# Optimization experiments

Measured on AMD Instinct MI355X. Metric: run time of the kernel, lower is better.

The kernel has to match this reference:

```python
import jax, jax.numpy as jnp
import numpy as np


def setup_inputs() -> dict:
    key = jax.random.key(0)
    k1, k2 = jax.random.split(key)
    z = jax.random.normal(k1, (16, 128, 32, 32), dtype=jnp.float32)
    e = jax.random.normal(k2, (8192, 128), dtype=jnp.float32)
    log_sigma = jnp.zeros((1,), dtype=jnp.float32)  # init_log_sigma = 0.0
    return {"z": z, "e": e, "log_sigma": log_sigma}


def reference(z, e, log_sigma):
    # z: [B, C, H, W] latents; e: [M, C] codebook; log_sigma: [1]
    B, C, H, W = z.shape
    zf = jnp.transpose(z, (0, 2, 3, 1)).reshape(-1, C)  # [N, C]
    N = zf.shape[0]
    M = e.shape[0]
    T = 1.0  # latent_temp default

    # squared L2 distance via expanded dot products: ||z||^2 + ||e||^2 - 2 z.e
    z_sq = jnp.sum(zf * zf, axis=1, keepdims=True)          # [N, 1]
    e_sq = jnp.sum(e * e, axis=1)[None, :]                  # [1, M]
    dist = jnp.maximum(z_sq + e_sq - 2.0 * (zf @ e.T), 0.0)  # [N, M]

    alpha = -1.0 / (2.0 * jnp.exp(log_sigma[0]) ** 2)
    A = alpha * dist / T                                     # [N, M]

    # np.log(np.e) == 1.0 in the original
    const = 0.5 * C * (2.0 * log_sigma - 1.0)                # [1]
    lse1_loss = -jnp.mean(T * jax.nn.logsumexp(A, axis=1)) + const + jnp.log(float(M))
    lse2_loss = -jnp.mean(T * jax.nn.logsumexp(A, axis=0)) + const + jnp.log(float(N))
    return lse1_loss, lse2_loss
```

## Files before the change

### kernel.cpp

```cpp
#include <hip/hip_runtime.h>
#include <hip/hip_bf16.h>

typedef unsigned short u16;
typedef __attribute__((ext_vector_type(8))) short short8;
typedef __attribute__((ext_vector_type(4))) float float4v;

#define N_ROWS 16384
#define M_COLS 8192
#define KDIM   128
#define SHIFT  64.0f

__device__ inline u16 f2bf(float f) {
  unsigned u = __builtin_bit_cast(unsigned, f);
  unsigned r = (u + 0x7fffu + ((u >> 16) & 1u)) >> 16;
  return (u16)r;
}

__global__ void prep_z(const float* __restrict__ z, u16* __restrict__ zf,
                       float* __restrict__ zsq) {
  const int b = blockIdx.x >> 5, h = blockIdx.x & 31;
  __shared__ float tile[128 * 33];
  __shared__ float psum[8][32];
  const float* src = z + ((size_t)b * 128 * 32 + h) * 32;
  for (int idx = threadIdx.x; idx < 4096; idx += 256) {
    int c = idx >> 5, w = idx & 31;
    tile[c * 33 + w] = src[c * 1024 + w];
  }
  __syncthreads();
  {
    int w = threadIdx.x & 31, cg = threadIdx.x >> 5;
    float s = 0.f;
#pragma unroll
    for (int cc = 0; cc < 16; ++cc) {
      float v = tile[(cg * 16 + cc) * 33 + w];
      s = fmaf(v, v, s);
    }
    psum[cg][w] = s;
  }
  for (int idx = threadIdx.x; idx < 512; idx += 256) {
    int w = idx >> 4, g = idx & 15;
    short8 v;
#pragma unroll
    for (int cc = 0; cc < 8; ++cc) v[cc] = (short)f2bf(tile[(g * 8 + cc) * 33 + w]);
    *(short8*)&zf[((size_t)b * 1024 + h * 32 + w) * 128 + g * 8] = v;
  }
  __syncthreads();
  if (threadIdx.x < 32) {
    int w = threadIdx.x;
    float s = 0.f;
#pragma unroll
    for (int cg = 0; cg < 8; ++cg) s += psum[cg][w];
    zsq[b * 1024 + h * 32 + w] = s;
  }
}

__global__ void prep_e(const float* __restrict__ e, u16* __restrict__ ef,
                       float* __restrict__ esq) {
  const int gw = (blockIdx.x * 256 + threadIdx.x) >> 6;
  const int ln = threadIdx.x & 63;
  for (int r = gw; r < M_COLS; r += 256) {
    float2 v = *(const float2*)&e[r * 128 + ln * 2];
    unsigned pk = (unsigned)f2bf(v.x) | ((unsigned)f2bf(v.y) << 16);
    *(unsigned*)&ef[r * 128 + ln * 2] = pk;
    float s = fmaf(v.x, v.x, v.y * v.y);
#pragma unroll
    for (int sh = 1; sh < 64; sh <<= 1) s += __shfl_xor(s, sh);
    if (ln == 0) esq[r] = s;
  }
}

__global__ __launch_bounds__(1024, 4) void gemm_lse(
    const u16* __restrict__ zf, const u16* __restrict__ ef,
    const float* __restrict__ zsq, const float* __restrict__ esq,
    const float* __restrict__ log_sigma,
    float* __restrict__ rowsum, float* __restrict__ colsum) {
  __shared__ __align__(16) u16 zt[256 * 128];
  __shared__ __align__(16) u16 et[256 * 128];
  const int tid = threadIdx.x;
  const int ln = tid & 63, wv = tid >> 6;
  const int wr = wv >> 2, wc = wv & 3;
  const int l15 = ln & 15, q = ln >> 4;
  const int bx = blockIdx.x, by = blockIdx.y;

  const u16* zsrc = zf + (size_t)by * (256 * 128);
  const u16* esrc = ef + (size_t)bx * (256 * 128);
#pragma unroll
  for (int it = 0; it < 4; ++it) {
    int u = it * 1024 + tid;
    int r = u >> 4, p = u & 15;
    int g = p ^ (r & 15);
    int soff = r * 128 + g * 8;
    int lbase = (it * 1024 + wv * 64) * 8;
    __builtin_amdgcn_global_load_lds(
        (const __attribute__((address_space(1))) unsigned int*)(zsrc + soff),
        (__attribute__((address_space(3))) unsigned int*)(zt + lbase), 16, 0, 0);
    __builtin_amdgcn_global_load_lds(
        (const __attribute__((address_space(1))) unsigned int*)(esrc + soff),
        (__attribute__((address_space(3))) unsigned int*)(et + lbase), 16, 0, 0);
  }

  float4v acc[4][4];
#pragma unroll
  for (int i = 0; i < 4; ++i)
#pragma unroll
    for (int j = 0; j < 4; ++j) acc[i][j] = (float4v){0.f, 0.f, 0.f, 0.f};

  __syncthreads();

#pragma unroll
  for (int kk = 0; kk < 4; ++kk) {
    short8 af[4], bfr[4];
    const int poff = ((kk * 4 + q) ^ l15) * 8;
#pragma unroll
    for (int i = 0; i < 4; ++i)
      af[i] = *(const short8*)(zt + (wr * 64 + i * 16 + l15) * 128 + poff);
#pragma unroll
    for (int j = 0; j < 4; ++j)
      bfr[j] = *(const short8*)(et + (wc * 64 + j * 16 + l15) * 128 + poff);
#pragma unroll
    for (int i = 0; i < 4; ++i)
#pragma unroll
      for (int j = 0; j < 4; ++j)
        acc[i][j] = __builtin_amdgcn_mfma_f32_16x16x32_bf16(af[i], bfr[j], acc[i][j], 0, 0, 0);
  }

  const float lsv = log_sigma[0];
  const float sg = __expf(lsv);
  const float alpha = -0.5f / (sg * sg);
  const float L2E = 1.44269504088896f;
  const float ca = alpha * L2E, cb = SHIFT * L2E, m2ca = -2.0f * ca;

  float4v zb[4];
  float eb[4];
#pragma unroll
  for (int i = 0; i < 4; ++i) {
    float4v zs = *(const float4v*)(zsq + by * 256 + wr * 64 + i * 16 + q * 4);
#pragma unroll
    for (int r = 0; r < 4; ++r) zb[i][r] = fmaf(ca, zs[r], cb);
  }
#pragma unroll
  for (int j = 0; j < 4; ++j) eb[j] = ca * esq[bx * 256 + wc * 64 + j * 16 + l15];

  float rs[4][4] = {};
  float cs[4] = {};
#pragma unroll
  for (int i = 0; i < 4; ++i) {
#pragma unroll
    for (int j = 0; j < 4; ++j) {
      float ex0, ex1, ex2, ex3;
      {
        float arg = fmaf(acc[i][j][0], m2ca, zb[i][0] + eb[j]);
        ex0 = __builtin_amdgcn_exp2f(arg);
      }
      {
        float arg = fmaf(acc[i][j][1], m2ca, zb[i][1] + eb[j]);
        ex1 = __builtin_amdgcn_exp2f(arg);
      }
      {
        float arg = fmaf(acc[i][j][2], m2ca, zb[i][2] + eb[j]);
        ex2 = __builtin_amdgcn_exp2f(arg);
      }
      {
        float arg = fmaf(acc[i][j][3], m2ca, zb[i][3] + eb[j]);
        ex3 = __builtin_amdgcn_exp2f(arg);
      }
      rs[i][0] += ex0; rs[i][1] += ex1; rs[i][2] += ex2; rs[i][3] += ex3;
      cs[j] += (ex0 + ex1) + (ex2 + ex3);
    }
  }
#pragma unroll
  for (int i = 0; i < 4; ++i)
#pragma unroll
    for (int r = 0; r < 4; ++r)
      for (int s = 1; s < 16; s <<= 1) rs[i][r] += __shfl_xor(rs[i][r], s);
#pragma unroll
  for (int j = 0; j < 4; ++j) {
    cs[j] += __shfl_xor(cs[j], 16);
    cs[j] += __shfl_xor(cs[j], 32);
  }

  __syncthreads();
  float* rbuf = (float*)zt;
  float* cbuf = rbuf + 1024;
  if (l15 == 0) {
#pragma unroll
    for (int i = 0; i < 4; ++i)
#pragma unroll
      for (int r = 0; r < 4; ++r)
        rbuf[wc * 256 + wr * 64 + i * 16 + q * 4 + r] = rs[i][r];
  }
  if (q == 0) {
#pragma unroll
    for (int j = 0; j < 4; ++j)
      cbuf[wr * 256 + wc * 64 + j * 16 + l15] = cs[j];
  }
  __syncthreads();
  if (tid < 256) {
    atomicAdd(&rowsum[by * 256 + tid],
              (rbuf[tid] + rbuf[256 + tid]) + (rbuf[512 + tid] + rbuf[768 + tid]));
  } else if (tid < 512) {
    int t = tid - 256;
    atomicAdd(&colsum[bx * 256 + t],
              (cbuf[t] + cbuf[256 + t]) + (cbuf[512 + t] + cbuf[768 + t]));
  }
}

__global__ void finalize(const float* __restrict__ rowsum, const float* __restrict__ colsum,
                         const float* __restrict__ log_sigma, float* __restrict__ out) {
  const int tid = threadIdx.x;
  const bool rows = (blockIdx.x == 0);
  const int n = rows ? N_ROWS : M_COLS;
  const float* buf = rows ? rowsum : colsum;
  double part = 0.0;
  for (int i = tid; i < n; i += 1024) part += (double)logf(buf[i]);
  __shared__ double red[1024];
  red[tid] = part;
  __syncthreads();
  for (int s = 512; s > 0; s >>= 1) {
    if (tid < s) red[tid] += red[tid + s];
    __syncthreads();
  }
  if (tid == 0) {
    float lsv = log_sigma[0];
    float cst = 0.5f * 128.0f * (2.0f * lsv - 1.0f);
    float lother = rows ? logf((float)M_COLS) : logf((float)N_ROWS);
    out[blockIdx.x] = (float)(-(red[0] / n - (double)SHIFT)) + cst + lother;
  }
}

extern "C" void kernel_launch(void* const* d_in, const int* in_sizes, int n_in,
                              void* d_out, int out_size, void* d_ws, size_t ws_size,
                              hipStream_t stream) {
  const float* z  = (const float*)d_in[0];
  const float* e  = (const float*)d_in[1];
  const float* ls = (const float*)d_in[2];
  float* out = (float*)d_out;
  char* ws = (char*)d_ws;
  u16*  zf     = (u16*)ws;
  u16*  ef     = (u16*)(ws + (4u << 20));
  float* zsq   = (float*)(ws + (6u << 20));
  float* esq   = (float*)(ws + (6u << 20) + 65536);
  float* rowsum = (float*)(ws + (6u << 20) + 65536 + 32768);
  float* colsum = (float*)(ws + (6u << 20) + 65536 + 32768 + 65536);

  hipMemsetAsync(rowsum, 0, 65536 + 32768, stream);
  prep_z<<<dim3(512), dim3(256), 0, stream>>>(z, zf, zsq);
  prep_e<<<dim3(64), dim3(256), 0, stream>>>(e, ef, esq);
  gemm_lse<<<dim3(32, 64), dim3(1024), 0, stream>>>(zf, ef, zsq, esq, ls, rowsum, colsum);
  finalize<<<dim3(2), dim3(1024), 0, stream>>>(rowsum, colsum, ls, out);
}
```

Measured before the change: 169.4 us.

## Restructure GEMM-LSE into register-resident z stripes with double-buffered codebook tiles

The two prep kernels are merged into one launch. The main kernel now keeps each block's 256 z rows in registers and streams 64-column codebook tiles through double-buffered LDS using async global-to-LDS loads. Global atomics and the memset are replaced by per-split row partials and per-stripe column partials, which a two-stage finalize reduces. This gives 512 blocks of 256 threads instead of 2048 blocks of 1024 threads, trading parallelism for operand reuse and less atomic traffic. It adds larger partial buffers and an extra kernel launch.

Measured after the change: 151.7 us. 10.4% less time.

```diff
diff --git a/kernel.cpp b/kernel.cpp
--- a/kernel.cpp
+++ b/kernel.cpp
@@ -9,6 +9,9 @@
 #define M_COLS 8192
 #define KDIM   128
 #define SHIFT  64.0f
+#define STRIPES 64
+#define SPLITS  8
+#define TILES   16
 
 __device__ inline u16 f2bf(float f) {
   unsigned u = __builtin_bit_cast(unsigned, f);
@@ -16,113 +19,81 @@
   return (u16)r;
 }
 
-__global__ void prep_z(const float* __restrict__ z, u16* __restrict__ zf,
-                       float* __restrict__ zsq) {
-  const int b = blockIdx.x >> 5, h = blockIdx.x & 31;
-  __shared__ float tile[128 * 33];
-  __shared__ float psum[8][32];
-  const float* src = z + ((size_t)b * 128 * 32 + h) * 32;
-  for (int idx = threadIdx.x; idx < 4096; idx += 256) {
-    int c = idx >> 5, w = idx & 31;
-    tile[c * 33 + w] = src[c * 1024 + w];
-  }
-  __syncthreads();
-  {
-    int w = threadIdx.x & 31, cg = threadIdx.x >> 5;
-    float s = 0.f;
-#pragma unroll
-    for (int cc = 0; cc < 16; ++cc) {
-      float v = tile[(cg * 16 + cc) * 33 + w];
-      s = fmaf(v, v, s);
-    }
-    psum[cg][w] = s;
-  }
-  for (int idx = threadIdx.x; idx < 512; idx += 256) {
-    int w = idx >> 4, g = idx & 15;
-    short8 v;
-#pragma unroll
-    for (int cc = 0; cc < 8; ++cc) v[cc] = (short)f2bf(tile[(g * 8 + cc) * 33 + w]);
-    *(short8*)&zf[((size_t)b * 1024 + h * 32 + w) * 128 + g * 8] = v;
-  }
-  __syncthreads();
-  if (threadIdx.x < 32) {
-    int w = threadIdx.x;
-    float s = 0.f;
-#pragma unroll
-    for (int cg = 0; cg < 8; ++cg) s += psum[cg][w];
-    zsq[b * 1024 + h * 32 + w] = s;
-  }
-}
-
-__global__ void prep_e(const float* __restrict__ e, u16* __restrict__ ef,
-                       float* __restrict__ esq) {
-  const int gw = (blockIdx.x * 256 + threadIdx.x) >> 6;
-  const int ln = threadIdx.x & 63;
-  for (int r = gw; r < M_COLS; r += 256) {
-    float2 v = *(const float2*)&e[r * 128 + ln * 2];
-    unsigned pk = (unsigned)f2bf(v.x) | ((unsigned)f2bf(v.y) << 16);
-    *(unsigned*)&ef[r * 128 + ln * 2] = pk;
-    float s = fmaf(v.x, v.x, v.y * v.y);
-#pragma unroll
-    for (int sh = 1; sh < 64; sh <<= 1) s += __shfl_xor(s, sh);
-    if (ln == 0) esq[r] = s;
-  }
-}
-
-__global__ __launch_bounds__(1024, 4) void gemm_lse(
+__global__ void prep(const float* __restrict__ z, const float* __restrict__ e,
+                     u16* __restrict__ zf, u16* __restrict__ ef,
+                     float* __restrict__ zsq, float* __restrict__ esq) {
+  if (blockIdx.x < 512) {
+    const int b = blockIdx.x >> 5, h = blockIdx.x & 31;
+    __shared__ float tile[128 * 33];
+    __shared__ float psum[8][32];
+    const float* src = z + ((size_t)b * 128 * 32 + h) * 32;
+    for (int idx = threadIdx.x; idx < 4096; idx += 256) {
+      int c = idx >> 5, w = idx & 31;
+      tile[c * 33 + w] = src[c * 1024 + w];
+    }
+    __syncthreads();
+    {
+      int w = threadIdx.x & 31, cg = threadIdx.x >> 5;
+      float s = 0.f;
+#pragma unroll
+      for (int cc = 0; cc < 16; ++cc) {
+        float v = tile[(cg * 16 + cc) * 33 + w];
+        s = fmaf(v, v, s);
+      }
+      psum[cg][w] = s;
+    }
+    for (int idx = threadIdx.x; idx < 512; idx += 256) {
+      int w = idx >> 4, g = idx & 15;
+      short8 v;
+#pragma unroll
+      for (int cc = 0; cc < 8; ++cc) v[cc] = (short)f2bf(tile[(g * 8 + cc) * 33 + w]);
+      *(short8*)&zf[((size_t)b * 1024 + h * 32 + w) * 128 + g * 8] = v;
+    }
+    __syncthreads();
+    if (threadIdx.x < 32) {
+      int w = threadIdx.x;
+      float s = 0.f;
+#pragma unroll
+      for (int cg = 0; cg < 8; ++cg) s += psum[cg][w];
+      zsq[b * 1024 + h * 32 + w] = s;
+    }
+  } else {
+    const int gw = ((blockIdx.x - 512) * 256 + threadIdx.x) >> 6;
+    const int ln = threadIdx.x & 63;
+    for (int r = gw; r < M_COLS; r += 256) {
+      float2 v = *(const float2*)&e[r * 128 + ln * 2];
+      unsigned pk = (unsigned)f2bf(v.x) | ((unsigned)f2bf(v.y) << 16);
+      *(unsigned*)&ef[r * 128 + ln * 2] = pk;
+      float s = fmaf(v.x, v.x, v.y * v.y);
+#pragma unroll
+      for (int sh = 1; sh < 64; sh <<= 1) s += __shfl_xor(s, sh);
+      if (ln == 0) esq[r] = s;
+    }
+  }
+}
+
+__global__ __launch_bounds__(256, 2) void gemm_lse(
     const u16* __restrict__ zf, const u16* __restrict__ ef,
     const float* __restrict__ zsq, const float* __restrict__ esq,
     const float* __restrict__ log_sigma,
-    float* __restrict__ rowsum, float* __restrict__ colsum) {
-  __shared__ __align__(16) u16 zt[256 * 128];
-  __shared__ __align__(16) u16 et[256 * 128];
+    float* __restrict__ rpart, float* __restrict__ cpart) {
+  __shared__ __align__(16) u16 et[2][64 * 128];
+  __shared__ float colacc[1024];
   const int tid = threadIdx.x;
   const int ln = tid & 63, wv = tid >> 6;
-  const int wr = wv >> 2, wc = wv & 3;
   const int l15 = ln & 15, q = ln >> 4;
-  const int bx = blockIdx.x, by = blockIdx.y;
-
-  const u16* zsrc = zf + (size_t)by * (256 * 128);
-  const u16* esrc = ef + (size_t)bx * (256 * 128);
-#pragma unroll
-  for (int it = 0; it < 4; ++it) {
-    int u = it * 1024 + tid;
-    int r = u >> 4, p = u & 15;
-    int g = p ^ (r & 15);
-    int soff = r * 128 + g * 8;
-    int lbase = (it * 1024 + wv * 64) * 8;
-    __builtin_amdgcn_global_load_lds(
-        (const __attribute__((address_space(1))) unsigned int*)(zsrc + soff),
-        (__attribute__((address_space(3))) unsigned int*)(zt + lbase), 16, 0, 0);
-    __builtin_amdgcn_global_load_lds(
-        (const __attribute__((address_space(1))) unsigned int*)(esrc + soff),
-        (__attribute__((address_space(3))) unsigned int*)(et + lbase), 16, 0, 0);
-  }
-
-  float4v acc[4][4];
+  const int stripe = blockIdx.x, split = blockIdx.y;
+  const int colbase = split * 1024;
+
+  for (int i = tid; i < 1024; i += 256) colacc[i] = 0.f;
+
+  short8 af[4][4];
 #pragma unroll
   for (int i = 0; i < 4; ++i)
 #pragma unroll
-    for (int j = 0; j < 4; ++j) acc[i][j] = (float4v){0.f, 0.f, 0.f, 0.f};
-
-  __syncthreads();
-
-#pragma unroll
-  for (int kk = 0; kk < 4; ++kk) {
-    short8 af[4], bfr[4];
-    const int poff = ((kk * 4 + q) ^ l15) * 8;
-#pragma unroll
-    for (int i = 0; i < 4; ++i)
-      af[i] = *(const short8*)(zt + (wr * 64 + i * 16 + l15) * 128 + poff);
-#pragma unroll
-    for (int j = 0; j < 4; ++j)
-      bfr[j] = *(const short8*)(et + (wc * 64 + j * 16 + l15) * 128 + poff);
-#pragma unroll
-    for (int i = 0; i < 4; ++i)
-#pragma unroll
-      for (int j = 0; j < 4; ++j)
-        acc[i][j] = __builtin_amdgcn_mfma_f32_16x16x32_bf16(af[i], bfr[j], acc[i][j], 0, 0, 0);
-  }
+    for (int kk = 0; kk < 4; ++kk)
+      af[i][kk] = *(const short8*)(zf +
+          (size_t)(stripe * 256 + wv * 64 + i * 16 + l15) * 128 + kk * 32 + q * 8);
 
   const float lsv = log_sigma[0];
   const float sg = __expf(lsv);
@@ -130,101 +101,164 @@
   const float L2E = 1.44269504088896f;
   const float ca = alpha * L2E, cb = SHIFT * L2E, m2ca = -2.0f * ca;
 
-  float4v zb[4];
-  float eb[4];
+  float4v zbl[4];
 #pragma unroll
   for (int i = 0; i < 4; ++i) {
-    float4v zs = *(const float4v*)(zsq + by * 256 + wr * 64 + i * 16 + q * 4);
-#pragma unroll
-    for (int r = 0; r < 4; ++r) zb[i][r] = fmaf(ca, zs[r], cb);
-  }
-#pragma unroll
-  for (int j = 0; j < 4; ++j) eb[j] = ca * esq[bx * 256 + wc * 64 + j * 16 + l15];
-
-  float rs[4][4] = {};
-  float cs[4] = {};
-#pragma unroll
-  for (int i = 0; i < 4; ++i) {
+    float4v zs = *(const float4v*)(zsq + stripe * 256 + wv * 64 + i * 16 + q * 4);
+#pragma unroll
+    for (int r = 0; r < 4; ++r) zbl[i][r] = fmaf(ca, zs[r], cb);
+  }
+
+  float2 rs2[4][2];
+#pragma unroll
+  for (int i = 0; i < 4; ++i)
+#pragma unroll
+    for (int p = 0; p < 2; ++p) rs2[i][p] = make_float2(0.f, 0.f);
+
+#define STAGE(tt)                                                              \
+  do {                                                                         \
+    const u16* efb = ef + (size_t)(colbase + (tt) * 64) * 128;                 \
+    u16* dstb = et[(tt) & 1];                                                  \
+    _Pragma("unroll")                                                          \
+    for (int it = 0; it < 4; ++it) {                                           \
+      int u = it * 256 + tid;                                                  \
+      int r = u >> 4, p_ = u & 15;                                             \
+      int g = p_ ^ (r & 15);                                                   \
+      __builtin_amdgcn_global_load_lds(                                        \
+          (const __attribute__((address_space(1))) unsigned int*)(efb + r * 128 + g * 8), \
+          (__attribute__((address_space(3))) unsigned int*)(dstb + (it * 256 + wv * 64) * 8), \
+          16, 0, 0);                                                           \
+    }                                                                          \
+  } while (0)
+
+  STAGE(0);
+
+  for (int t = 0; t < TILES; ++t) {
+    __syncthreads();
+    const u16* bb = et[t & 1];
+
+    float4v acc[4][4];
+#pragma unroll
+    for (int kk = 0; kk < 4; ++kk) {
+      short8 bfr[4];
+      const int poff = ((kk * 4 + q) ^ l15) * 8;
+#pragma unroll
+      for (int j = 0; j < 4; ++j)
+        bfr[j] = *(const short8*)(bb + (j * 16 + l15) * 128 + poff);
+      if (kk == 0) {
+#pragma unroll
+        for (int i = 0; i < 4; ++i)
+#pragma unroll
+          for (int j = 0; j < 4; ++j)
+            acc[i][j] = __builtin_amdgcn_mfma_f32_16x16x32_bf16(
+                af[i][0], bfr[j], (float4v){0.f, 0.f, 0.f, 0.f}, 0, 0, 0);
+      } else {
+#pragma unroll
+        for (int i = 0; i < 4; ++i)
+#pragma unroll
+          for (int j = 0; j < 4; ++j)
+            acc[i][j] = __builtin_amdgcn_mfma_f32_16x16x32_bf16(
+                af[i][kk], bfr[j], acc[i][j], 0, 0, 0);
+      }
+    }
+
+    if (t + 1 < TILES) STAGE(t + 1);
+
+    float ebv[4];
+#pragma unroll
+    for (int j = 0; j < 4; ++j) ebv[j] = ca * esq[colbase + t * 64 + j * 16 + l15];
+
+    float2 cs2[4];
+#pragma unroll
+    for (int j = 0; j < 4; ++j) cs2[j] = make_float2(0.f, 0.f);
+
+#pragma unroll
+    for (int i = 0; i < 4; ++i) {
+#pragma unroll
+      for (int j = 0; j < 4; ++j) {
+        float e0 = __builtin_amdgcn_exp2f(fmaf(acc[i][j][0], m2ca, zbl[i][0] + ebv[j]));
+        float e1 = __builtin_amdgcn_exp2f(fmaf(acc[i][j][1], m2ca, zbl[i][1] + ebv[j]));
+        float e2 = __builtin_amdgcn_exp2f(fmaf(acc[i][j][2], m2ca, zbl[i][2] + ebv[j]));
+        float e3 = __builtin_amdgcn_exp2f(fmaf(acc[i][j][3], m2ca, zbl[i][3] + ebv[j]));
+        rs2[i][0].x += e0; rs2[i][0].y += e1;
+        rs2[i][1].x += e2; rs2[i][1].y += e3;
+        cs2[j].x += e0 + e2; cs2[j].y += e1 + e3;
+      }
+    }
 #pragma unroll
     for (int j = 0; j < 4; ++j) {
-      float ex0, ex1, ex2, ex3;
-      {
-        float arg = fmaf(acc[i][j][0], m2ca, zb[i][0] + eb[j]);
-        ex0 = __builtin_amdgcn_exp2f(arg);
-      }
-      {
-        float arg = fmaf(acc[i][j][1], m2ca, zb[i][1] + eb[j]);
-        ex1 = __builtin_amdgcn_exp2f(arg);
-      }
-      {
-        float arg = fmaf(acc[i][j][2], m2ca, zb[i][2] + eb[j]);
-        ex2 = __builtin_amdgcn_exp2f(arg);
-      }
-      {
-        float arg = fmaf(acc[i][j][3], m2ca, zb[i][3] + eb[j]);
-        ex3 = __builtin_amdgcn_exp2f(arg);
-      }
-      rs[i][0] += ex0; rs[i][1] += ex1; rs[i][2] += ex2; rs[i][3] += ex3;
-      cs[j] += (ex0 + ex1) + (ex2 + ex3);
-    }
-  }
+      float c = cs2[j].x + cs2[j].y;
+      c += __shfl_xor(c, 16);
+      c += __shfl_xor(c, 32);
+      if (q == 0) atomicAdd(&colacc[t * 64 + j * 16 + l15], c);
+    }
+  }
+
+  __syncthreads();
+  for (int i = tid; i < 1024; i += 256)
+    cpart[(size_t)stripe * 8192 + colbase + i] = colacc[i];
+
 #pragma unroll
   for (int i = 0; i < 4; ++i)
 #pragma unroll
-    for (int r = 0; r < 4; ++r)
-      for (int s = 1; s < 16; s <<= 1) rs[i][r] += __shfl_xor(rs[i][r], s);
-#pragma unroll
-  for (int j = 0; j < 4; ++j) {
-    cs[j] += __shfl_xor(cs[j], 16);
-    cs[j] += __shfl_xor(cs[j], 32);
-  }
-
+    for (int p = 0; p < 2; ++p)
+      for (int s = 1; s < 16; s <<= 1) {
+        rs2[i][p].x += __shfl_xor(rs2[i][p].x, s);
+        rs2[i][p].y += __shfl_xor(rs2[i][p].y, s);
+      }
+  if (l15 == 0) {
+#pragma unroll
+    for (int i = 0; i < 4; ++i) {
+      int rbase = (size_t)0 + stripe * 256 + wv * 64 + i * 16 + q * 4;
+      rpart[(size_t)split * N_ROWS + rbase + 0] = rs2[i][0].x;
+      rpart[(size_t)split * N_ROWS + rbase + 1] = rs2[i][0].y;
+      rpart[(size_t)split * N_ROWS + rbase + 2] = rs2[i][1].x;
+      rpart[(size_t)split * N_ROWS + rbase + 3] = rs2[i][1].y;
+    }
+  }
+#undef STAGE
+}
+
+__global__ void fin1(const float* __restrict__ rpart, const float* __restrict__ cpart,
+                     double* __restrict__ lpart) {
+  const int tid = threadIdx.x, b = blockIdx.x;
+  double v;
+  if (b < 64) {
+    int row = b * 256 + tid;
+    float s = 0.f;
+#pragma unroll
+    for (int p = 0; p < SPLITS; ++p) s += rpart[(size_t)p * N_ROWS + row];
+    v = (double)logf(s);
+  } else {
+    int col = (b - 64) * 256 + tid;
+    float s = 0.f;
+#pragma unroll
+    for (int p = 0; p < STRIPES; ++p) s += cpart[(size_t)p * M_COLS + col];
+    v = (double)logf(s);
+  }
+  __shared__ double red[256];
+  red[tid] = v;
   __syncthreads();
-  float* rbuf = (float*)zt;
-  float* cbuf = rbuf + 1024;
-  if (l15 == 0) {
-#pragma unroll
-    for (int i = 0; i < 4; ++i)
-#pragma unroll
-      for (int r = 0; r < 4; ++r)
-        rbuf[wc * 256 + wr * 64 + i * 16 + q * 4 + r] = rs[i][r];
-  }
-  if (q == 0) {
-#pragma unroll
-    for (int j = 0; j < 4; ++j)
-      cbuf[wr * 256 + wc * 64 + j * 16 + l15] = cs[j];
-  }
-  __syncthreads();
-  if (tid < 256) {
-    atomicAdd(&rowsum[by * 256 + tid],
-              (rbuf[tid] + rbuf[256 + tid]) + (rbuf[512 + tid] + rbuf[768 + tid]));
-  } else if (tid < 512) {
-    int t = tid - 256;
-    atomicAdd(&colsum[bx * 256 + t],
-              (cbuf[t] + cbuf[256 + t]) + (cbuf[512 + t] + cbuf[768 + t]));
-  }
-}
-
-__global__ void finalize(const float* __restrict__ rowsum, const float* __restrict__ colsum,
-                         const float* __restrict__ log_sigma, float* __restrict__ out) {
+  for (int s = 128; s > 0; s >>= 1) {
+    if (tid < s) red[tid] += red[tid + s];
+    __syncthreads();
+  }
+  if (tid == 0) lpart[b] = red[0];
+}
+
+__global__ void fin2(const double* __restrict__ lpart,
+                     const float* __restrict__ log_sigma, float* __restrict__ out) {
   const int tid = threadIdx.x;
-  const bool rows = (blockIdx.x == 0);
-  const int n = rows ? N_ROWS : M_COLS;
-  const float* buf = rows ? rowsum : colsum;
-  double part = 0.0;
-  for (int i = tid; i < n; i += 1024) part += (double)logf(buf[i]);
-  __shared__ double red[1024];
-  red[tid] = part;
-  __syncthreads();
-  for (int s = 512; s > 0; s >>= 1) {
-    if (tid < s) red[tid] += red[tid + s];
-    __syncthreads();
-  }
+  float lsv = log_sigma[0];
+  float cst = 0.5f * 128.0f * (2.0f * lsv - 1.0f);
   if (tid == 0) {
-    float lsv = log_sigma[0];
-    float cst = 0.5f * 128.0f * (2.0f * lsv - 1.0f);
-    float lother = rows ? logf((float)M_COLS) : logf((float)N_ROWS);
-    out[blockIdx.x] = (float)(-(red[0] / n - (double)SHIFT)) + cst + lother;
+    double s = 0.0;
+    for (int i = 0; i < 64; ++i) s += lpart[i];
+    out[0] = (float)(-(s / N_ROWS - (double)SHIFT)) + cst + logf((float)M_COLS);
+  } else if (tid == 1) {
+    double s = 0.0;
+    for (int i = 64; i < 96; ++i) s += lpart[i];
+    out[1] = (float)(-(s / M_COLS - (double)SHIFT)) + cst + logf((float)N_ROWS);
   }
 }
 
@@ -236,16 +270,16 @@
   const float* ls = (const float*)d_in[2];
   float* out = (float*)d_out;
   char* ws = (char*)d_ws;
-  u16*  zf     = (u16*)ws;
-  u16*  ef     = (u16*)(ws + (4u << 20));
+  u16*   zf    = (u16*)ws;
+  u16*   ef    = (u16*)(ws + (4u << 20));
   float* zsq   = (float*)(ws + (6u << 20));
-  float* esq   = (float*)(ws + (6u << 20) + 65536);
-  float* rowsum = (float*)(ws + (6u << 20) + 65536 + 32768);
-  float* colsum = (float*)(ws + (6u << 20) + 65536 + 32768 + 65536);
-
-  hipMemsetAsync(rowsum, 0, 65536 + 32768, stream);
-  prep_z<<<dim3(512), dim3(256), 0, stream>>>(z, zf, zsq);
-  prep_e<<<dim3(64), dim3(256), 0, stream>>>(e, ef, esq);
-  gemm_lse<<<dim3(32, 64), dim3(1024), 0, stream>>>(zf, ef, zsq, esq, ls, rowsum, colsum);
-  finalize<<<dim3(2), dim3(1024), 0, stream>>>(rowsum, colsum, ls, out);
-}
+  float* esq   = (float*)(ws + (6u << 20) + (64u << 10));
+  float* rpart = (float*)(ws + (6u << 20) + (96u << 10));
+  float* cpart = (float*)(ws + (6u << 20) + (608u << 10));
+  double* lpart = (double*)(ws + (6u << 20) + (608u << 10) + (2u << 20));
+
+  prep<<<dim3(576), dim3(256), 0, stream>>>(z, e, zf, ef, zsq, esq);
+  gemm_lse<<<dim3(STRIPES, SPLITS), dim3(256), 0, stream>>>(zf, ef, zsq, esq, ls, rpart, cpart);
+  fin1<<<dim3(96), dim3(256), 0, stream>>>(rpart, cpart, lpart);
+  fin2<<<dim3(1), dim3(64), 0, stream>>>(lpart, ls, out);
+}
```
